# Optimization experiments

Measured on AMD Instinct MI355X. Metric: run time of the kernel, lower is better.

The kernel has to match this reference:

```python
import math
import jax, jax.numpy as jnp
import numpy as np

S, B, H = 2048, 1, 4096
NH, HD = 32, 128          # heads, head dim
ROT = HD // 2             # rotary dim per 2D-RoPE half = 64


def rotate_half(x):
    x1, x2 = jnp.split(x, 2, axis=-1)
    return jnp.concatenate([-x2, x1], axis=-1)


def rope_tables(seq_len, dim, base=10000.0):
    inv_freq = 1.0 / (base ** (jnp.arange(0, dim, 2, dtype=jnp.float32) / dim))
    freqs = jnp.arange(seq_len, dtype=jnp.float32)[:, None] * inv_freq[None, :]
    emb = jnp.concatenate([freqs, freqs], axis=-1)  # [S, dim]
    return jnp.cos(emb), jnp.sin(emb)


def apply_rope(q, k, cos, sin, pos):
    # q,k: [S,B,NH,ROT]; pos: [S,B] -> gather cos/sin per token
    c = cos[pos][:, :, None, :]  # [S,B,1,ROT]
    s = sin[pos][:, :, None, :]
    return q * c + rotate_half(q) * s, k * c + rotate_half(k) * s


def setup_inputs() -> dict:
    key = jax.random.key(0)
    ks = jax.random.split(key, 5)
    hidden_states = jax.random.normal(ks[0], (S, B, H), dtype=jnp.float32)
    pos = jnp.arange(S, dtype=jnp.int64 if jax.config.jax_enable_x64 else jnp.int32)
    position_ids = jnp.stack([pos, pos])[None]  # [B=1, 2, S]
    attention_mask = jnp.triu(jnp.ones((S, S), dtype=bool), k=1)[None, None]  # True = masked
    scale = 0.02
    wqkv = jax.random.normal(ks[1], (3 * H, H), dtype=jnp.float32) * scale
    bqkv = jax.random.normal(ks[2], (3 * H,), dtype=jnp.float32) * scale
    wdense = jax.random.normal(ks[3], (H, H), dtype=jnp.float32) * scale
    bdense = jax.random.normal(ks[4], (H,), dtype=jnp.float32) * scale
    return {"hidden_states": hidden_states, "position_ids": position_ids,
            "attention_mask": attention_mask, "wqkv": wqkv, "bqkv": bqkv,
            "wdense": wdense, "bdense": bdense, "layer_id": 1}


def reference(hidden_states, position_ids, attention_mask, wqkv, bqkv, wdense, bdense, layer_id):
    s, b, h = hidden_states.shape
    # fused QKV projection: [S,B,NH,3*HD]
    mixed = (jnp.einsum('sbh,oh->sbo', hidden_states, wqkv) + bqkv).reshape(s, b, NH, 3 * HD)
    q, k, v = jnp.split(mixed, 3, axis=-1)  # each [S,B,NH,HD]

    # 2D RoPE: split head dim in half, rotate each half with its own position ids
    q1, q2 = jnp.split(q, 2, axis=-1)
    k1, k2 = jnp.split(k, 2, axis=-1)
    cos, sin = rope_tables(s, ROT)
    pos = position_ids[:, 0, :].T       # [S,B]
    block_pos = position_ids[:, 1, :].T  # [S,B]
    q1, k1 = apply_rope(q1, k1, cos, sin, pos)
    q2, k2 = apply_rope(q2, k2, cos, sin, block_pos)
    q = jnp.concatenate([q1, q2], axis=-1)
    k = jnp.concatenate([k1, k2], axis=-1)

    # layer-scaled attention (ChatGLM style)
    coeff = float(layer_id + 1)
    q = q / (math.sqrt(HD) * coeff)
    scores = jnp.einsum('sbhd,tbhd->bhst', q, k)  # [B,NH,S,S]
    scores = jnp.where(attention_mask, jnp.float32(-10000.0), scores)
    scores = scores.astype(jnp.float32) * coeff
    probs = jax.nn.softmax(scores, axis=-1).astype(q.dtype)
    context = jnp.einsum('bhst,tbhd->sbhd', probs, v).reshape(s, b, h)

    out = jnp.einsum('sbh,oh->sbo', context, wdense) + bdense
    return out
```

## Files before the change

kernel.cpp:

```cpp
#include <hip/hip_runtime.h>

typedef unsigned short u16;
typedef unsigned int u32;
typedef __attribute__((ext_vector_type(4))) float f32x4;
typedef __attribute__((ext_vector_type(8))) short bf16x8;
typedef __attribute__((ext_vector_type(2))) unsigned int u32x2;

#define S_LEN 2048
#define NHEAD 32
#define HDD 128
#define HID 4096
#define N_QKV 12288
#define KDIM 4096
#define RS 12288

__device__ __forceinline__ u16 f2bf(float f) {
  u32 u = __builtin_bit_cast(u32, f);
  u = (u + 0x7FFFu + ((u >> 16) & 1u)) >> 16;
  return (u16)u;
}
__device__ __forceinline__ float bf2f(u16 h) {
  u32 u = ((u32)h) << 16;
  return __builtin_bit_cast(float, u);
}

__device__ __forceinline__ void gl2lds16(const void* g, void* l) {
  __builtin_amdgcn_global_load_lds(
      (const __attribute__((address_space(1))) u32*)g,
      (__attribute__((address_space(3))) u32*)l, 16, 0, 0);
}

#define FULL_BAR()                          \
  {                                         \
    asm volatile("" ::: "memory");          \
    __builtin_amdgcn_s_barrier();           \
    asm volatile("" ::: "memory");          \
  }

__global__ __launch_bounds__(256) void cvt3_kernel(const float* __restrict__ s0, u16* __restrict__ d0, int n0,
                                                   const float* __restrict__ s1, u16* __restrict__ d1, int n1,
                                                   const float* __restrict__ s2, u16* __restrict__ d2, int n2) {
  int i = blockIdx.x * blockDim.x + threadIdx.x;
  int st = gridDim.x * blockDim.x;
  int ntot = n0 + n1 + n2;
  for (; i < ntot; i += st) {
    const float* s;
    u16* d;
    int j = i;
    if (j < n0) {
      s = s0; d = d0;
    } else if (j < n0 + n1) {
      j -= n0; s = s1; d = d1;
    } else {
      j -= n0 + n1; s = s2; d = d2;
    }
    float4 v = ((const float4*)s)[j];
    u32x2 o;
    o.x = (u32)f2bf(v.x) | ((u32)f2bf(v.y) << 16);
    o.y = (u32)f2bf(v.z) | ((u32)f2bf(v.w) << 16);
    ((u32x2*)d)[j] = o;
  }
}

__global__ __launch_bounds__(256) void tables_kernel(float* __restrict__ cos_t,
                                                     float* __restrict__ sin_t) {
  int idx = blockIdx.x * blockDim.x + threadIdx.x;
  if (idx >= S_LEN * 32) return;
  int s = idx >> 5, i = idx & 31;
  float invf = expf(-0.28782313662425572f * (float)i);
  float a = (float)s * invf;
  cos_t[idx] = cosf(a);
  sin_t[idx] = sinf(a);
}

__global__ __launch_bounds__(256) void rope_kernel(u16* __restrict__ mixed,
                                                   const int* __restrict__ pid,
                                                   const float* __restrict__ cos_t,
                                                   const float* __restrict__ sin_t) {
  int idx = blockIdx.x * blockDim.x + threadIdx.x;
  const int total = 2 * NHEAD * S_LEN * 2 * 8;
  if (idx >= total) return;
  int j = idx & 7;
  int half = (idx >> 3) & 1;
  int s = (idx >> 4) & (S_LEN - 1);
  int h = (idx >> 15) & (NHEAD - 1);
  int qk = idx >> 20;
  int i0 = j * 4;
  int p = pid[half * S_LEN + s];
  float4 c4 = *(const float4*)(cos_t + p * 32 + i0);
  float4 s4 = *(const float4*)(sin_t + p * 32 + i0);
  u16* base = mixed + (size_t)s * RS + h * 384 + qk * 128 + half * 64 + i0;
  ushort4 x1v = *(const ushort4*)(base);
  ushort4 x2v = *(const ushort4*)(base + 32);
  float sc = qk ? 1.0f : 0.08838834764831845f;
  ushort4 o1, o2;
  {
    float x1 = bf2f(x1v.x), x2 = bf2f(x2v.x);
    o1.x = f2bf((x1 * c4.x - x2 * s4.x) * sc);
    o2.x = f2bf((x2 * c4.x + x1 * s4.x) * sc);
  }
  {
    float x1 = bf2f(x1v.y), x2 = bf2f(x2v.y);
    o1.y = f2bf((x1 * c4.y - x2 * s4.y) * sc);
    o2.y = f2bf((x2 * c4.y + x1 * s4.y) * sc);
  }
  {
    float x1 = bf2f(x1v.z), x2 = bf2f(x2v.z);
    o1.z = f2bf((x1 * c4.z - x2 * s4.z) * sc);
    o2.z = f2bf((x2 * c4.z + x1 * s4.z) * sc);
  }
  {
    float x1 = bf2f(x1v.w), x2 = bf2f(x2v.w);
    o1.w = f2bf((x1 * c4.w - x2 * s4.w) * sc);
    o2.w = f2bf((x2 * c4.w + x1 * s4.w) * sc);
  }
  *(ushort4*)(base) = o1;
  *(ushort4*)(base + 32) = o2;
}

template <int NW, int EPI>
__global__ __launch_bounds__(512, 2) void gemmK(const u16* __restrict__ A,
                                                const u16* __restrict__ B,
                                                const float* __restrict__ bias, int N, int NTt,
                                                u16* __restrict__ outb, float* __restrict__ outf) {
  constexpr int BN = 32 * NW;
  constexpr int NLB = NW / 2;
  constexpr int BSUB = BN * 64;
  constexpr int BUFSZ = 32768 + 2 * BSUB;
  constexpr int NH2 = NW / 2;
  __shared__ __align__(16) char lds[2][BUFSZ];

  const int tid = threadIdx.x;
  const int lane = tid & 63, w = tid >> 6;
  const int l15 = lane & 15, g = lane >> 4;
  const int wm = w >> 1, wn = w & 1;

  int perx = gridDim.x >> 3;
  int npx = perx >> 3;
  int x = blockIdx.x & 7, loc = blockIdx.x >> 3;
  int mb = loc & 7, nb = x * npx + (loc >> 3);
  const int bm = mb * 256, bn = nb * BN;

  f32x4 acc[4][NW];
  f32x4 z4 = {0.f, 0.f, 0.f, 0.f};
#pragma unroll
  for (int mi = 0; mi < 4; ++mi)
#pragma unroll
    for (int ni = 0; ni < NW; ++ni) acc[mi][ni] = z4;

  const size_t K2 = (size_t)KDIM * 2;

  const char* gA[2];
#pragma unroll
  for (int j = 0; j < 2; ++j) {
    int slot = j * 512 + tid;
    int line = slot >> 3;
    int sl = (slot & 7) ^ (line & 7);
    int row = 2 * line + (sl >> 2);
    int colb = (sl & 3) * 16;
    gA[j] = (const char*)A + (size_t)(bm + row) * K2 + colb;
  }
  const char* gB[NLB];
#pragma unroll
  for (int j = 0; j < NLB; ++j) {
    int n_ = j * 512 + tid;
    int kkj = (n_ >= 128 * NW) ? 1 : 0;
    int m_ = n_ - kkj * 128 * NW;
    int line = m_ >> 3;
    int sl = (m_ & 7) ^ (line & 7);
    int row = 2 * line + (sl >> 2);
    int colb = (sl & 3) * 16;
    gB[j] = (const char*)B + (size_t)(bn + row) * K2 + kkj * 64 + colb;
  }
  const int ldst = w * 1024;

#define ISSUE_A(t, kk)                                                        \
  {                                                                           \
    char* Lb = lds[(t) & 1] + (kk) * 16384;                                   \
    gl2lds16(gA[0] + (size_t)(t) * 128 + (kk) * 64, Lb + ldst);               \
    gl2lds16(gA[1] + (size_t)(t) * 128 + (kk) * 64, Lb + 8192 + ldst);        \
  }
#define ISSUE_B(t)                                                            \
  {                                                                           \
    char* Lb = lds[(t) & 1] + 32768;                                          \
    _Pragma("unroll")                                                         \
    for (int j = 0; j < NLB; ++j)                                             \
      gl2lds16(gB[j] + (size_t)(t) * 128, Lb + j * 8192 + ldst);              \
  }

  int offA[4], offB[2][NW];
#pragma unroll
  for (int mi = 0; mi < 4; ++mi) {
    int r = wm * 64 + mi * 16 + l15;
    int line = r >> 1;
    int sl = (((r & 1) << 2) + g) ^ (line & 7);
    offA[mi] = line * 128 + sl * 16;
  }
#pragma unroll
  for (int kk = 0; kk < 2; ++kk)
#pragma unroll
    for (int ni = 0; ni < NW; ++ni) {
      int r = wn * (16 * NW) + ni * 16 + l15;
      int line = r >> 1;
      int sl = (((r & 1) << 2) + g) ^ (line & 7);
      offB[kk][ni] = 32768 + kk * BSUB + line * 128 + sl * 16;
    }

  ISSUE_A(0, 0);
  ISSUE_B(0);
  ISSUE_A(0, 1);
  asm volatile("s_waitcnt vmcnt(0)" ::: "memory");
  FULL_BAR();

  for (int kt = 0; kt < NTt; ++kt) {
    const char* buf = lds[kt & 1];
    const bool pf = (kt + 1) < NTt;
    bf16x8 a[4], b[NH2];
#pragma unroll
    for (int mi = 0; mi < 4; ++mi) a[mi] = *(const bf16x8*)(buf + offA[mi]);
#pragma unroll
    for (int ni = 0; ni < NH2; ++ni) b[ni] = *(const bf16x8*)(buf + offB[0][ni]);
    if (pf) ISSUE_A(kt + 1, 0);
    FULL_BAR();
    __builtin_amdgcn_s_setprio(1);
#pragma unroll
    for (int mi = 0; mi < 4; ++mi)
#pragma unroll
      for (int ni = 0; ni < NH2; ++ni)
        acc[mi][ni] = __builtin_amdgcn_mfma_f32_16x16x32_bf16(a[mi], b[ni], acc[mi][ni], 0, 0, 0);
    __builtin_amdgcn_s_setprio(0);
#pragma unroll
    for (int ni = 0; ni < NH2; ++ni) b[ni] = *(const bf16x8*)(buf + offB[0][NH2 + ni]);
    if (pf) ISSUE_B(kt + 1);
    if (pf) {
      asm volatile("s_waitcnt vmcnt(%0)" ::"i"(2 + NLB) : "memory");
    } else {
      asm volatile("s_waitcnt vmcnt(0)" ::: "memory");
    }
    FULL_BAR();
    __builtin_amdgcn_s_setprio(1);
#pragma unroll
    for (int mi = 0; mi < 4; ++mi)
#pragma unroll
      for (int ni = 0; ni < NH2; ++ni)
        acc[mi][NH2 + ni] = __builtin_amdgcn_mfma_f32_16x16x32_bf16(a[mi], b[ni], acc[mi][NH2 + ni], 0, 0, 0);
    __builtin_amdgcn_s_setprio(0);
#pragma unroll
    for (int mi = 0; mi < 4; ++mi) a[mi] = *(const bf16x8*)(buf + 16384 + offA[mi]);
#pragma unroll
    for (int ni = 0; ni < NH2; ++ni) b[ni] = *(const bf16x8*)(buf + offB[1][ni]);
    if (pf) ISSUE_A(kt + 1, 1);
    FULL_BAR();
    __builtin_amdgcn_s_setprio(1);
#pragma unroll
    for (int mi = 0; mi < 4; ++mi)
#pragma unroll
      for (int ni = 0; ni < NH2; ++ni)
        acc[mi][ni] = __builtin_amdgcn_mfma_f32_16x16x32_bf16(a[mi], b[ni], acc[mi][ni], 0, 0, 0);
    __builtin_amdgcn_s_setprio(0);
#pragma unroll
    for (int ni = 0; ni < NH2; ++ni) b[ni] = *(const bf16x8*)(buf + offB[1][NH2 + ni]);
    if (pf) asm volatile("s_waitcnt vmcnt(2)" ::: "memory");
    FULL_BAR();
    __builtin_amdgcn_s_setprio(1);
#pragma unroll
    for (int mi = 0; mi < 4; ++mi)
#pragma unroll
      for (int ni = 0; ni < NH2; ++ni)
        acc[mi][NH2 + ni] = __builtin_amdgcn_mfma_f32_16x16x32_bf16(a[mi], b[ni], acc[mi][NH2 + ni], 0, 0, 0);
    __builtin_amdgcn_s_setprio(0);
  }
#undef ISSUE_A
#undef ISSUE_B

#pragma unroll
  for (int ni = 0; ni < NW; ++ni) {
    int n = bn + wn * (16 * NW) + ni * 16 + l15;
    float bv = bias[n];
    if (EPI == 0) {
#pragma unroll
      for (int mi = 0; mi < 4; ++mi) {
        int m0 = bm + wm * 64 + mi * 16 + 4 * g;
#pragma unroll
        for (int rr = 0; rr < 4; ++rr)
          outb[(size_t)(m0 + rr) * N + n] = f2bf(acc[mi][ni][rr] + bv);
      }
    } else {
#pragma unroll
      for (int mi = 0; mi < 4; ++mi) {
        int m0 = bm + wm * 64 + mi * 16 + 4 * g;
#pragma unroll
        for (int rr = 0; rr < 4; ++rr) outf[(size_t)(m0 + rr) * N + n] = acc[mi][ni][rr] + bv;
      }
    }
  }
}

__global__ __launch_bounds__(256) void attn_kernel(const u16* __restrict__ mixed,
                                                   u16* __restrict__ ctx) {
  __shared__ __align__(16) u16 Ksh[32 * 136];
  __shared__ __align__(16) u16 Vsh[128 * 32];
  __shared__ __align__(16) u16 Pt[4][16 * 40];

  int tid = threadIdx.x;
  int lane = tid & 63, w = tid >> 6;
  int lane15 = lane & 15, g = lane >> 4;

  int i = blockIdx.x;
  int qb_base = i & 7;
  int h = (i >> 3) & 31;
  int quarter = i >> 8;
  int qbi = (quarter == 0) ? qb_base
            : (quarter == 1) ? (15 - qb_base)
            : (quarter == 2) ? (16 + qb_base)
                             : (31 - qb_base);
  int qbase = qbi * 64;
  int qrow = qbase + w * 16 + lane15;

  const u16* qp = mixed + (size_t)h * 384;
  const u16* kp = mixed + (size_t)h * 384 + 128;
  const u16* vp = mixed + (size_t)h * 384 + 256;

  bf16x8 qf[4];
  const u16* qptr = qp + (size_t)qrow * RS + g * 8;
#pragma unroll
  for (int d0 = 0; d0 < 4; ++d0) qf[d0] = *(const bf16x8*)(qptr + d0 * 32);

  f32x4 pv[8];
  f32x4 z4 = {0.f, 0.f, 0.f, 0.f};
#pragma unroll
  for (int db = 0; db < 8; ++db) pv[db] = z4;
  float m_run = -1e30f, l_run = 0.0f;

  int krow = tid >> 3, kc = (tid & 7) * 16;
  int a_ = tid & 15, b_ = tid >> 4;
  int ntiles = (qbase >> 5) + 2;

  for (int t = 0; t < ntiles; ++t) {
    int kb0 = t * 32;
    __syncthreads();
    {
      const bf16x8* src = (const bf16x8*)(kp + (size_t)(kb0 + krow) * RS + kc);
      bf16x8 x0 = src[0], x1 = src[1];
      *(bf16x8*)(Ksh + krow * 136 + kc) = x0;
      *(bf16x8*)(Ksh + krow * 136 + kc + 8) = x1;
      int k0 = 2 * a_, d0 = 8 * b_;
      bf16x8 r0 = *(const bf16x8*)(vp + (size_t)(kb0 + k0) * RS + d0);
      bf16x8 r1 = *(const bf16x8*)(vp + (size_t)(kb0 + k0 + 1) * RS + d0);
#pragma unroll
      for (int jj = 0; jj < 8; ++jj) {
        int d = d0 + jj;
        u32 val = (u32)(u16)r0[jj] | ((u32)(u16)r1[jj] << 16);
        *(u32*)(Vsh + d * 32 + (((k0 >> 3) ^ (d & 3)) << 3) + (k0 & 7)) = val;
      }
    }
    __syncthreads();

    f32x4 sa0 = z4, sa1 = z4;
#pragma unroll
    for (int d0 = 0; d0 < 4; ++d0) {
      bf16x8 k0f = *(const bf16x8*)(Ksh + lane15 * 136 + d0 * 32 + g * 8);
      bf16x8 k1f = *(const bf16x8*)(Ksh + (16 + lane15) * 136 + d0 * 32 + g * 8);
      sa0 = __builtin_amdgcn_mfma_f32_16x16x32_bf16(k0f, qf[d0], sa0, 0, 0, 0);
      sa1 = __builtin_amdgcn_mfma_f32_16x16x32_bf16(k1f, qf[d0], sa1, 0, 0, 0);
    }
    float s[8];
#pragma unroll
    for (int rr = 0; rr < 4; ++rr) {
      int kg0 = kb0 + 4 * g + rr;
      int kg1 = kb0 + 16 + 4 * g + rr;
      s[rr] = (kg0 > qrow) ? -1e30f : sa0[rr];
      s[4 + rr] = (kg1 > qrow) ? -1e30f : sa1[rr];
    }
    float mx = s[0];
#pragma unroll
    for (int i2 = 1; i2 < 8; ++i2) mx = fmaxf(mx, s[i2]);
    mx = fmaxf(mx, __shfl_xor(mx, 16));
    mx = fmaxf(mx, __shfl_xor(mx, 32));
    float mnew = fmaxf(m_run, mx);
    float fac = exp2f((m_run - mnew) * 1.4426950408889634f);
    float p[8], psum = 0.f;
#pragma unroll
    for (int i2 = 0; i2 < 8; ++i2) {
      p[i2] = exp2f((s[i2] - mnew) * 1.4426950408889634f);
      psum += p[i2];
    }
    psum += __shfl_xor(psum, 16);
    psum += __shfl_xor(psum, 32);
    l_run = l_run * fac + psum;
    m_run = mnew;
#pragma unroll
    for (int db = 0; db < 8; ++db) pv[db] *= fac;

    u32 w0 = (u32)f2bf(p[0]) | ((u32)f2bf(p[1]) << 16);
    u32 w1 = (u32)f2bf(p[2]) | ((u32)f2bf(p[3]) << 16);
    u32 w2 = (u32)f2bf(p[4]) | ((u32)f2bf(p[5]) << 16);
    u32 w3 = (u32)f2bf(p[6]) | ((u32)f2bf(p[7]) << 16);
    u32x2 pa, pb;
    pa.x = w0; pa.y = w1; pb.x = w2; pb.y = w3;
    *(u32x2*)(&Pt[w][lane15 * 40 + 4 * g]) = pa;
    *(u32x2*)(&Pt[w][lane15 * 40 + 16 + 4 * g]) = pb;
    asm volatile("s_waitcnt lgkmcnt(0)" ::: "memory");
    bf16x8 pfrag = *(const bf16x8*)(&Pt[w][lane15 * 40 + 8 * g]);

#pragma unroll
    for (int db = 0; db < 8; ++db) {
      int d = db * 16 + lane15;
      bf16x8 vf = *(const bf16x8*)(Vsh + d * 32 + ((g ^ (d & 3)) << 3));
      pv[db] = __builtin_amdgcn_mfma_f32_16x16x32_bf16(vf, pfrag, pv[db], 0, 0, 0);
    }
  }

  float inv = 1.0f / l_run;
#pragma unroll
  for (int db = 0; db < 8; ++db) {
    ushort4 o;
    o.x = f2bf(pv[db][0] * inv);
    o.y = f2bf(pv[db][1] * inv);
    o.z = f2bf(pv[db][2] * inv);
    o.w = f2bf(pv[db][3] * inv);
    *(ushort4*)(ctx + (size_t)qrow * HID + h * HDD + db * 16 + 4 * g) = o;
  }
}

extern "C" void kernel_launch(void* const* d_in, const int* in_sizes, int n_in,
                              void* d_out, int out_size, void* d_ws, size_t ws_size,
                              hipStream_t stream) {
  const float* hidden = (const float*)d_in[0];
  const int* pid = (const int*)d_in[1];
  const float* wqkv = (const float*)d_in[3];
  const float* bqkv = (const float*)d_in[4];
  const float* wdense = (const float*)d_in[5];
  const float* bdense = (const float*)d_in[6];
  float* out = (float*)d_out;

  char* ws = (char*)d_ws;
  u16* W1 = (u16*)ws;
  u16* W2 = (u16*)(ws + 100663296);
  u16* X = (u16*)(ws + 134217728);
  u16* mixed = (u16*)(ws + 150994944);
  u16* ctx = (u16*)(ws + 201326592);
  float* cos_t = (float*)(ws + 218103808);
  float* sin_t = (float*)(ws + 218365952);

  cvt3_kernel<<<dim3(2048), dim3(256), 0, stream>>>(
      wqkv, W1, N_QKV * KDIM / 4, wdense, W2, HID * KDIM / 4, hidden, X, S_LEN * HID / 4);
  tables_kernel<<<dim3(256), dim3(256), 0, stream>>>(cos_t, sin_t);

  gemmK<6, 0><<<dim3(512), dim3(512), 0, stream>>>(
      X, W1, bqkv, N_QKV, 64, mixed, nullptr);

  rope_kernel<<<dim3(8192), dim3(256), 0, stream>>>(mixed, pid, cos_t, sin_t);

  attn_kernel<<<dim3(1024), dim3(256), 0, stream>>>(mixed, ctx);

  gemmK<4, 1><<<dim3(256), dim3(512), 0, stream>>>(
      ctx, W2, bdense, HID, 64, nullptr, out);
}
```

Measured before the change: 497.8 us.

## Merge RoPE table build into convert kernel, restructure GEMM k-loop, pair attention query blocks

```diff
diff --git a/kernel.cpp b/kernel.cpp
--- a/kernel.cpp
+++ b/kernel.cpp
@@ -39,8 +39,16 @@
 
 __global__ __launch_bounds__(256) void cvt3_kernel(const float* __restrict__ s0, u16* __restrict__ d0, int n0,
                                                    const float* __restrict__ s1, u16* __restrict__ d1, int n1,
-                                                   const float* __restrict__ s2, u16* __restrict__ d2, int n2) {
+                                                   const float* __restrict__ s2, u16* __restrict__ d2, int n2,
+                                                   float* __restrict__ cos_t, float* __restrict__ sin_t) {
   int i = blockIdx.x * blockDim.x + threadIdx.x;
+  if (i < S_LEN * 32) {
+    int s = i >> 5, ii = i & 31;
+    float invf = expf(-0.28782313662425572f * (float)ii);
+    float a = (float)s * invf;
+    cos_t[i] = cosf(a);
+    sin_t[i] = sinf(a);
+  }
   int st = gridDim.x * blockDim.x;
   int ntot = n0 + n1 + n2;
   for (; i < ntot; i += st) {
@@ -60,17 +68,6 @@
     o.y = (u32)f2bf(v.z) | ((u32)f2bf(v.w) << 16);
     ((u32x2*)d)[j] = o;
   }
-}
-
-__global__ __launch_bounds__(256) void tables_kernel(float* __restrict__ cos_t,
-                                                     float* __restrict__ sin_t) {
-  int idx = blockIdx.x * blockDim.x + threadIdx.x;
-  if (idx >= S_LEN * 32) return;
-  int s = idx >> 5, i = idx & 31;
-  float invf = expf(-0.28782313662425572f * (float)i);
-  float a = (float)s * invf;
-  cos_t[idx] = cosf(a);
-  sin_t[idx] = sinf(a);
 }
 
 __global__ __launch_bounds__(256) void rope_kernel(u16* __restrict__ mixed,
@@ -127,7 +124,6 @@
   constexpr int NLB = NW / 2;
   constexpr int BSUB = BN * 64;
   constexpr int BUFSZ = 32768 + 2 * BSUB;
-  constexpr int NH2 = NW / 2;
   __shared__ __align__(16) char lds[2][BUFSZ];
 
   const int tid = threadIdx.x;
@@ -209,30 +205,20 @@
   ISSUE_A(0, 0);
   ISSUE_B(0);
   ISSUE_A(0, 1);
-  asm volatile("s_waitcnt vmcnt(0)" ::: "memory");
+  asm volatile("s_waitcnt vmcnt(2)" ::: "memory");
   FULL_BAR();
 
   for (int kt = 0; kt < NTt; ++kt) {
     const char* buf = lds[kt & 1];
     const bool pf = (kt + 1) < NTt;
-    bf16x8 a[4], b[NH2];
+    bf16x8 a[4], b[NW];
 #pragma unroll
     for (int mi = 0; mi < 4; ++mi) a[mi] = *(const bf16x8*)(buf + offA[mi]);
 #pragma unroll
-    for (int ni = 0; ni < NH2; ++ni) b[ni] = *(const bf16x8*)(buf + offB[0][ni]);
-    if (pf) ISSUE_A(kt + 1, 0);
-    FULL_BAR();
-    __builtin_amdgcn_s_setprio(1);
-#pragma unroll
-    for (int mi = 0; mi < 4; ++mi)
-#pragma unroll
-      for (int ni = 0; ni < NH2; ++ni)
-        acc[mi][ni] = __builtin_amdgcn_mfma_f32_16x16x32_bf16(a[mi], b[ni], acc[mi][ni], 0, 0, 0);
-    __builtin_amdgcn_s_setprio(0);
-#pragma unroll
-    for (int ni = 0; ni < NH2; ++ni) b[ni] = *(const bf16x8*)(buf + offB[0][NH2 + ni]);
-    if (pf) ISSUE_B(kt + 1);
+    for (int ni = 0; ni < NW; ++ni) b[ni] = *(const bf16x8*)(buf + offB[0][ni]);
     if (pf) {
+      ISSUE_A(kt + 1, 0);
+      ISSUE_B(kt + 1);
       asm volatile("s_waitcnt vmcnt(%0)" ::"i"(2 + NLB) : "memory");
     } else {
       asm volatile("s_waitcnt vmcnt(0)" ::: "memory");
@@ -242,32 +228,24 @@
 #pragma unroll
     for (int mi = 0; mi < 4; ++mi)
 #pragma unroll
-      for (int ni = 0; ni < NH2; ++ni)
-        acc[mi][NH2 + ni] = __builtin_amdgcn_mfma_f32_16x16x32_bf16(a[mi], b[ni], acc[mi][NH2 + ni], 0, 0, 0);
+      for (int ni = 0; ni < NW; ++ni)
+        acc[mi][ni] = __builtin_amdgcn_mfma_f32_16x16x32_bf16(a[mi], b[ni], acc[mi][ni], 0, 0, 0);
     __builtin_amdgcn_s_setprio(0);
 #pragma unroll
     for (int mi = 0; mi < 4; ++mi) a[mi] = *(const bf16x8*)(buf + 16384 + offA[mi]);
 #pragma unroll
-    for (int ni = 0; ni < NH2; ++ni) b[ni] = *(const bf16x8*)(buf + offB[1][ni]);
-    if (pf) ISSUE_A(kt + 1, 1);
+    for (int ni = 0; ni < NW; ++ni) b[ni] = *(const bf16x8*)(buf + offB[1][ni]);
+    if (pf) {
+      ISSUE_A(kt + 1, 1);
+      asm volatile("s_waitcnt vmcnt(2)" ::: "memory");
+    }
     FULL_BAR();
     __builtin_amdgcn_s_setprio(1);
 #pragma unroll
     for (int mi = 0; mi < 4; ++mi)
 #pragma unroll
-      for (int ni = 0; ni < NH2; ++ni)
+      for (int ni = 0; ni < NW; ++ni)
         acc[mi][ni] = __builtin_amdgcn_mfma_f32_16x16x32_bf16(a[mi], b[ni], acc[mi][ni], 0, 0, 0);
-    __builtin_amdgcn_s_setprio(0);
-#pragma unroll
-    for (int ni = 0; ni < NH2; ++ni) b[ni] = *(const bf16x8*)(buf + offB[1][NH2 + ni]);
-    if (pf) asm volatile("s_waitcnt vmcnt(2)" ::: "memory");
-    FULL_BAR();
-    __builtin_amdgcn_s_setprio(1);
-#pragma unroll
-    for (int mi = 0; mi < 4; ++mi)
-#pragma unroll
-      for (int ni = 0; ni < NH2; ++ni)
-        acc[mi][NH2 + ni] = __builtin_amdgcn_mfma_f32_16x16x32_bf16(a[mi], b[ni], acc[mi][NH2 + ni], 0, 0, 0);
     __builtin_amdgcn_s_setprio(0);
   }
 #undef ISSUE_A
@@ -306,120 +284,119 @@
   int lane = tid & 63, w = tid >> 6;
   int lane15 = lane & 15, g = lane >> 4;
 
-  int i = blockIdx.x;
-  int qb_base = i & 7;
-  int h = (i >> 3) & 31;
-  int quarter = i >> 8;
-  int qbi = (quarter == 0) ? qb_base
-            : (quarter == 1) ? (15 - qb_base)
-            : (quarter == 2) ? (16 + qb_base)
-                             : (31 - qb_base);
-  int qbase = qbi * 64;
-  int qrow = qbase + w * 16 + lane15;
+  int bpair = blockIdx.x & 15;
+  int h = blockIdx.x >> 4;
 
   const u16* qp = mixed + (size_t)h * 384;
   const u16* kp = mixed + (size_t)h * 384 + 128;
   const u16* vp = mixed + (size_t)h * 384 + 256;
 
-  bf16x8 qf[4];
-  const u16* qptr = qp + (size_t)qrow * RS + g * 8;
-#pragma unroll
-  for (int d0 = 0; d0 < 4; ++d0) qf[d0] = *(const bf16x8*)(qptr + d0 * 32);
-
-  f32x4 pv[8];
-  f32x4 z4 = {0.f, 0.f, 0.f, 0.f};
-#pragma unroll
-  for (int db = 0; db < 8; ++db) pv[db] = z4;
-  float m_run = -1e30f, l_run = 0.0f;
-
   int krow = tid >> 3, kc = (tid & 7) * 16;
   int a_ = tid & 15, b_ = tid >> 4;
-  int ntiles = (qbase >> 5) + 2;
-
-  for (int t = 0; t < ntiles; ++t) {
-    int kb0 = t * 32;
+  f32x4 z4 = {0.f, 0.f, 0.f, 0.f};
+
+  for (int pass = 0; pass < 2; ++pass) {
+    int qi = pass ? (31 - bpair) : bpair;
+    int qbase = qi * 64;
+    int qrow = qbase + w * 16 + lane15;
+    int ntiles = 2 * qi + 2;
+
+    bf16x8 qf[4];
+    const u16* qptr = qp + (size_t)qrow * RS + g * 8;
+#pragma unroll
+    for (int d0 = 0; d0 < 4; ++d0) qf[d0] = *(const bf16x8*)(qptr + d0 * 32);
+
+    f32x4 pv[8];
+#pragma unroll
+    for (int db = 0; db < 8; ++db) pv[db] = z4;
+    float m_run = -1e30f, l_run = 0.0f;
+
+    for (int t = 0; t < ntiles; ++t) {
+      int kb0 = t * 32;
+      __syncthreads();
+      {
+        const bf16x8* src = (const bf16x8*)(kp + (size_t)(kb0 + krow) * RS + kc);
+        bf16x8 x0 = src[0], x1 = src[1];
+        *(bf16x8*)(Ksh + krow * 136 + kc) = x0;
+        *(bf16x8*)(Ksh + krow * 136 + kc + 8) = x1;
+        int k0 = 2 * a_, d0 = 8 * b_;
+        bf16x8 r0 = *(const bf16x8*)(vp + (size_t)(kb0 + k0) * RS + d0);
+        bf16x8 r1 = *(const bf16x8*)(vp + (size_t)(kb0 + k0 + 1) * RS + d0);
+#pragma unroll
+        for (int jj = 0; jj < 8; ++jj) {
+          int d = d0 + jj;
+          u32 val = (u32)(u16)r0[jj] | ((u32)(u16)r1[jj] << 16);
+          *(u32*)(Vsh + d * 32 + (((k0 >> 3) ^ (d & 3)) << 3) + (k0 & 7)) = val;
+        }
+      }
+      __syncthreads();
+
+      f32x4 sa0 = z4, sa1 = z4;
+#pragma unroll
+      for (int d0 = 0; d0 < 4; ++d0) {
+        bf16x8 k0f = *(const bf16x8*)(Ksh + lane15 * 136 + d0 * 32 + g * 8);
+        bf16x8 k1f = *(const bf16x8*)(Ksh + (16 + lane15) * 136 + d0 * 32 + g * 8);
+        sa0 = __builtin_amdgcn_mfma_f32_16x16x32_bf16(k0f, qf[d0], sa0, 0, 0, 0);
+        sa1 = __builtin_amdgcn_mfma_f32_16x16x32_bf16(k1f, qf[d0], sa1, 0, 0, 0);
+      }
+      float s[8];
+#pragma unroll
+      for (int rr = 0; rr < 4; ++rr) {
+        int kg0 = kb0 + 4 * g + rr;
+        int kg1 = kb0 + 16 + 4 * g + rr;
+        s[rr] = (kg0 > qrow) ? -1e30f : sa0[rr];
+        s[4 + rr] = (kg1 > qrow) ? -1e30f : sa1[rr];
+      }
+      float mx = s[0];
+#pragma unroll
+      for (int i2 = 1; i2 < 8; ++i2) mx = fmaxf(mx, s[i2]);
+      mx = fmaxf(mx, __shfl_xor(mx, 16));
+      mx = fmaxf(mx, __shfl_xor(mx, 32));
+      float mnew = fmaxf(m_run, mx);
+      float fac = exp2f((m_run - mnew) * 1.4426950408889634f);
+      float p[8], psum = 0.f;
+#pragma unroll
+      for (int i2 = 0; i2 < 8; ++i2) {
+        p[i2] = exp2f((s[i2] - mnew) * 1.4426950408889634f);
+        psum += p[i2];
+      }
+      psum += __shfl_xor(psum, 16);
+      psum += __shfl_xor(psum, 32);
+      l_run = l_run * fac + psum;
+      m_run = mnew;
+#pragma unroll
+      for (int db = 0; db < 8; ++db) pv[db] *= fac;
+
+      u32 w0 = (u32)f2bf(p[0]) | ((u32)f2bf(p[1]) << 16);
+      u32 w1 = (u32)f2bf(p[2]) | ((u32)f2bf(p[3]) << 16);
+      u32 w2 = (u32)f2bf(p[4]) | ((u32)f2bf(p[5]) << 16);
+      u32 w3 = (u32)f2bf(p[6]) | ((u32)f2bf(p[7]) << 16);
+      u32x2 pa, pb;
+      pa.x = w0; pa.y = w1; pb.x = w2; pb.y = w3;
+      *(u32x2*)(&Pt[w][lane15 * 40 + 4 * g]) = pa;
+      *(u32x2*)(&Pt[w][lane15 * 40 + 16 + 4 * g]) = pb;
+      asm volatile("s_waitcnt lgkmcnt(0)" ::: "memory");
+      bf16x8 pfrag = *(const bf16x8*)(&Pt[w][lane15 * 40 + 8 * g]);
+
+#pragma unroll
+      for (int db = 0; db < 8; ++db) {
+        int d = db * 16 + lane15;
+        bf16x8 vf = *(const bf16x8*)(Vsh + d * 32 + ((g ^ (d & 3)) << 3));
+        pv[db] = __builtin_amdgcn_mfma_f32_16x16x32_bf16(vf, pfrag, pv[db], 0, 0, 0);
+      }
+    }
+
+    float inv = 1.0f / l_run;
+#pragma unroll
+    for (int db = 0; db < 8; ++db) {
+      ushort4 o;
+      o.x = f2bf(pv[db][0] * inv);
+      o.y = f2bf(pv[db][1] * inv);
+      o.z = f2bf(pv[db][2] * inv);
+      o.w = f2bf(pv[db][3] * inv);
+      *(ushort4*)(ctx + (size_t)qrow * HID + h * HDD + db * 16 + 4 * g) = o;
+    }
     __syncthreads();
-    {
-      const bf16x8* src = (const bf16x8*)(kp + (size_t)(kb0 + krow) * RS + kc);
-      bf16x8 x0 = src[0], x1 = src[1];
-      *(bf16x8*)(Ksh + krow * 136 + kc) = x0;
-      *(bf16x8*)(Ksh + krow * 136 + kc + 8) = x1;
-      int k0 = 2 * a_, d0 = 8 * b_;
-      bf16x8 r0 = *(const bf16x8*)(vp + (size_t)(kb0 + k0) * RS + d0);
-      bf16x8 r1 = *(const bf16x8*)(vp + (size_t)(kb0 + k0 + 1) * RS + d0);
-#pragma unroll
-      for (int jj = 0; jj < 8; ++jj) {
-        int d = d0 + jj;
-        u32 val = (u32)(u16)r0[jj] | ((u32)(u16)r1[jj] << 16);
-        *(u32*)(Vsh + d * 32 + (((k0 >> 3) ^ (d & 3)) << 3) + (k0 & 7)) = val;
-      }
-    }
-    __syncthreads();
-
-    f32x4 sa0 = z4, sa1 = z4;
-#pragma unroll
-    for (int d0 = 0; d0 < 4; ++d0) {
-      bf16x8 k0f = *(const bf16x8*)(Ksh + lane15 * 136 + d0 * 32 + g * 8);
-      bf16x8 k1f = *(const bf16x8*)(Ksh + (16 + lane15) * 136 + d0 * 32 + g * 8);
-      sa0 = __builtin_amdgcn_mfma_f32_16x16x32_bf16(k0f, qf[d0], sa0, 0, 0, 0);
-      sa1 = __builtin_amdgcn_mfma_f32_16x16x32_bf16(k1f, qf[d0], sa1, 0, 0, 0);
-    }
-    float s[8];
-#pragma unroll
-    for (int rr = 0; rr < 4; ++rr) {
-      int kg0 = kb0 + 4 * g + rr;
-      int kg1 = kb0 + 16 + 4 * g + rr;
-      s[rr] = (kg0 > qrow) ? -1e30f : sa0[rr];
-      s[4 + rr] = (kg1 > qrow) ? -1e30f : sa1[rr];
-    }
-    float mx = s[0];
-#pragma unroll
-    for (int i2 = 1; i2 < 8; ++i2) mx = fmaxf(mx, s[i2]);
-    mx = fmaxf(mx, __shfl_xor(mx, 16));
-    mx = fmaxf(mx, __shfl_xor(mx, 32));
-    float mnew = fmaxf(m_run, mx);
-    float fac = exp2f((m_run - mnew) * 1.4426950408889634f);
-    float p[8], psum = 0.f;
-#pragma unroll
-    for (int i2 = 0; i2 < 8; ++i2) {
-      p[i2] = exp2f((s[i2] - mnew) * 1.4426950408889634f);
-      psum += p[i2];
-    }
-    psum += __shfl_xor(psum, 16);
-    psum += __shfl_xor(psum, 32);
-    l_run = l_run * fac + psum;
-    m_run = mnew;
-#pragma unroll
-    for (int db = 0; db < 8; ++db) pv[db] *= fac;
-
-    u32 w0 = (u32)f2bf(p[0]) | ((u32)f2bf(p[1]) << 16);
-    u32 w1 = (u32)f2bf(p[2]) | ((u32)f2bf(p[3]) << 16);
-    u32 w2 = (u32)f2bf(p[4]) | ((u32)f2bf(p[5]) << 16);
-    u32 w3 = (u32)f2bf(p[6]) | ((u32)f2bf(p[7]) << 16);
-    u32x2 pa, pb;
-    pa.x = w0; pa.y = w1; pb.x = w2; pb.y = w3;
-    *(u32x2*)(&Pt[w][lane15 * 40 + 4 * g]) = pa;
-    *(u32x2*)(&Pt[w][lane15 * 40 + 16 + 4 * g]) = pb;
-    asm volatile("s_waitcnt lgkmcnt(0)" ::: "memory");
-    bf16x8 pfrag = *(const bf16x8*)(&Pt[w][lane15 * 40 + 8 * g]);
-
-#pragma unroll
-    for (int db = 0; db < 8; ++db) {
-      int d = db * 16 + lane15;
-      bf16x8 vf = *(const bf16x8*)(Vsh + d * 32 + ((g ^ (d & 3)) << 3));
-      pv[db] = __builtin_amdgcn_mfma_f32_16x16x32_bf16(vf, pfrag, pv[db], 0, 0, 0);
-    }
-  }
-
-  float inv = 1.0f / l_run;
-#pragma unroll
-  for (int db = 0; db < 8; ++db) {
-    ushort4 o;
-    o.x = f2bf(pv[db][0] * inv);
-    o.y = f2bf(pv[db][1] * inv);
-    o.z = f2bf(pv[db][2] * inv);
-    o.w = f2bf(pv[db][3] * inv);
-    *(ushort4*)(ctx + (size_t)qrow * HID + h * HDD + db * 16 + 4 * g) = o;
   }
 }
 
@@ -444,15 +421,15 @@
   float* sin_t = (float*)(ws + 218365952);
 
   cvt3_kernel<<<dim3(2048), dim3(256), 0, stream>>>(
-      wqkv, W1, N_QKV * KDIM / 4, wdense, W2, HID * KDIM / 4, hidden, X, S_LEN * HID / 4);
-  tables_kernel<<<dim3(256), dim3(256), 0, stream>>>(cos_t, sin_t);
+      wqkv, W1, N_QKV * KDIM / 4, wdense, W2, HID * KDIM / 4, hidden, X, S_LEN * HID / 4,
+      cos_t, sin_t);
 
   gemmK<6, 0><<<dim3(512), dim3(512), 0, stream>>>(
       X, W1, bqkv, N_QKV, 64, mixed, nullptr);
 
   rope_kernel<<<dim3(8192), dim3(256), 0, stream>>>(mixed, pid, cos_t, sin_t);
 
-  attn_kernel<<<dim3(1024), dim3(256), 0, stream>>>(mixed, ctx);
+  attn_kernel<<<dim3(512), dim3(256), 0, stream>>>(mixed, ctx);
 
   gemmK<4, 1><<<dim3(256), dim3(512), 0, stream>>>(
       ctx, W2, bdense, HID, 64, nullptr, out);
```

After: 500.5 us. No clear change (+0.5%).
